# Kernel optimization log

Hardware: AMD Instinct MI355X
Metric: run time of the kernel (lower is better)

Reference implementation:

```python
import jax, jax.numpy as jnp
import numpy as np

RADIUS = 2.0  # ball-query radius (float forward arg in the original; fixed here)


def _conv1x1(x, W, b):
    # 1x1 Conv2D over NHWC == per-point linear layer
    return jnp.einsum('bmsc,cd->bmsd', x, W) + b


def _ball_query(xyz, new_xyz, radius, nsample):
    """For each cluster center, take the first (by index) nsample points within
    radius, padding with the first found neighbor (TF ball-query semantics).
    xyz: (B,N,3), new_xyz: (B,M,3) -> idx (B,M,nsample) int32."""
    N = xyz.shape[1]
    d2 = jnp.sum((new_xyz[:, :, None, :] - xyz[:, None, :, :]) ** 2, axis=-1)  # (B,M,N)
    valid = d2 < radius * radius
    key = jnp.where(valid, jnp.arange(N, dtype=jnp.int32)[None, None, :], N)
    order = jnp.argsort(key, axis=-1)[..., :nsample]          # (B,M,nsample)
    skey = jnp.take_along_axis(key, order, axis=-1)
    idx = jnp.where(skey < N, order, order[..., :1])          # pad with first neighbor
    return idx


def setup_inputs() -> dict:
    key = jax.random.key(0)
    ks = jax.random.split(key, 8)
    B, N = 8, 8192
    xyz = jax.random.normal(ks[0], (B, N, 3), dtype=jnp.float32)

    def w(k, cin, cout):
        return (jax.random.normal(k, (cin, cout), dtype=jnp.float32) / np.sqrt(cin)).astype(jnp.float32)

    z = lambda c: jnp.zeros((c,), jnp.float32)
    inp = {
        'xyz': xyz,
        'W1': w(ks[1], 3, 64),    'b1': z(64),
        'W2': w(ks[2], 64, 128),  'b2': z(128),
        'W3': w(ks[3], 128, 256), 'b3': z(256),
        'W4': w(ks[4], 256, 128), 'b4': z(128),
        'W5': w(ks[5], 128, 64),  'b5': z(64),
        'Wa': w(ks[6], 64, 1),    'ba': z(1),
        'Wo': w(ks[7], 64, 2),    'bo': z(2),
        'num_clusters': 512,
        'num_samples': 64,
    }
    return inp


def reference(xyz, W1, b1, W2, b2, W3, b3, W4, b4, W5, b5, Wa, ba, Wo, bo,
              num_clusters, num_samples):
    # sample cluster centers (deterministic stand-in for random subsampling)
    new_xyz = xyz[:, :num_clusters]                                    # (B,M,3)
    idx = _ball_query(xyz, new_xyz, RADIUS, num_samples)               # (B,M,S)
    grouped = jax.vmap(lambda pts, i: pts[i])(xyz, idx)                # (B,M,S,3)
    g = (grouped - new_xyz[:, :, None, :]) / RADIUS                    # normalize_radius

    # shared per-point MLP (1x1 convs, relu)
    h = jax.nn.relu(_conv1x1(g, W1, b1))
    h = jax.nn.relu(_conv1x1(h, W2, b2))
    h = jax.nn.relu(_conv1x1(h, W3, b3))
    # MaxPoolAxis: max over samples, keepdims
    h = jnp.max(h, axis=2, keepdims=True)                              # (B,M,1,256)
    # mlp2 convs (linear, no activation in source)
    h = _conv1x1(h, W4, b4)
    h = _conv1x1(h, W5, b5)                                            # (B,M,1,64)

    attention = jax.nn.softplus(_conv1x1(h, Wa, ba))[:, :, 0, 0]       # (B,M)
    o = _conv1x1(h, Wo, bo)[:, :, 0, :]                                # (B,M,2)
    o = o / jnp.sqrt(jnp.maximum(jnp.sum(o * o, axis=-1, keepdims=True), 1e-8))
    orientation = jnp.arctan2(o[..., 1], o[..., 0])                    # (B,M)
    return new_xyz, idx, attention, orientation
```

## Files before the change

### kernel.cpp

```cpp
#include <hip/hip_runtime.h>
#include <math.h>

#define BB 8
#define NN 8192
#define MM 512
#define SS 64
#define NCLUST (BB*MM)

#define OUT_IDX   (BB*MM*3)
#define OUT_ATT   (OUT_IDX + BB*MM*SS)
#define OUT_ORI   (OUT_ATT + BB*MM)

#define WS_W3 8192
#define WS_V  40960

typedef short v8s __attribute__((ext_vector_type(8)));
typedef float v4f __attribute__((ext_vector_type(4)));

static __device__ __forceinline__ unsigned short f2bf(float x) {
    unsigned int u = __float_as_uint(x);
    u += 0x7FFFu + ((u >> 16) & 1u);
    return (unsigned short)(u >> 16);
}

__global__ void pack_weights(const float* __restrict__ W2,
                             const float* __restrict__ W3,
                             unsigned short* __restrict__ ws)
{
    const int gid = blockIdx.x * 256 + threadIdx.x;
    const float* W; unsigned short* dst; int N, kt, nt, lane;
    if (gid < 1024) {
        W = W2; N = 128;
        const int tile = gid >> 6; lane = gid & 63;
        kt = tile >> 3; nt = tile & 7;
        dst = ws + (size_t)(tile * 64 + lane) * 8;
    } else {
        const int g = gid - 1024;
        W = W3; N = 256;
        const int tile = g >> 6; lane = g & 63;
        kt = tile >> 4; nt = tile & 15;
        dst = ws + WS_W3 + (size_t)(tile * 64 + lane) * 8;
    }
    const int k0 = kt * 32 + (lane >> 4) * 8;
    const int n  = nt * 16 + (lane & 15);
    union { unsigned short u[8]; v8s v; } f;
    #pragma unroll
    for (int j = 0; j < 8; ++j) f.u[j] = f2bf(W[(k0 + j) * N + n]);
    *(v8s*)dst = f.v;
}

__global__ __launch_bounds__(256, 4) void feat3d_front(
    const float* __restrict__ xyz,
    const float* __restrict__ W1, const float* __restrict__ b1,
    const float* __restrict__ b2, const float* __restrict__ b3,
    const unsigned short* __restrict__ Wp,
    unsigned short* __restrict__ vdst,
    float* __restrict__ out)
{
    __shared__ __align__(16) unsigned char lds[27200];
    unsigned short* a2p = (unsigned short*)lds;
    unsigned short* a3p = (unsigned short*)(lds + 8192);
    float* smallf       = (float*)(lds + 24576);
    int* ls_idx         = (int*)(lds + 26624);
    unsigned long long* ls_mask = (unsigned long long*)(lds + 26880);

    float* ls_g  = smallf;
    float* ls_w1 = smallf + 256;

    const int t   = threadIdx.x;
    const int wv  = t >> 6;
    const int l   = t & 63;
    const int q   = l >> 4;
    const int r16 = l & 15;
    const int blk = blockIdx.x;
    const int b   = blk >> 9;
    const int m   = blk & 511;
    const float* xb = xyz + (size_t)b * (NN * 3);

    const v8s* W2f = (const v8s*)Wp;
    v8s bfr[2][2];
    #pragma unroll
    for (int kt = 0; kt < 2; ++kt)
        #pragma unroll
        for (int ni = 0; ni < 2; ++ni)
            bfr[kt][ni] = W2f[(kt*8 + 2*wv + ni)*64 + l];

    const float cx = xb[m*3+0], cy = xb[m*3+1], cz = xb[m*3+2];

    if (t < 3) out[(b*MM + m)*3 + t] = xb[m*3 + t];

    if (t < 64) {
        ls_w1[t*4+0] = W1[t];
        ls_w1[t*4+1] = W1[64 + t];
        ls_w1[t*4+2] = W1[128 + t];
        ls_w1[t*4+3] = b1[t];
    }

    int cnt = 0;
    {
        int base = 0, pb = 0;
        while (base < NN && cnt < SS) {
            const int j = base + t;
            const float dx = xb[j*3+0] - cx;
            const float dy = xb[j*3+1] - cy;
            const float dz = xb[j*3+2] - cz;
            const float d2 = __fadd_rn(__fadd_rn(__fmul_rn(dx,dx), __fmul_rn(dy,dy)),
                                       __fmul_rn(dz,dz));
            const bool valid = d2 < 4.0f;
            const unsigned long long mask = __ballot(valid);
            if (l == 0) ls_mask[pb*4 + wv] = mask;
            __syncthreads();
            const unsigned long long m0 = ls_mask[pb*4+0], m1 = ls_mask[pb*4+1],
                                     m2 = ls_mask[pb*4+2], m3 = ls_mask[pb*4+3];
            int below = __popcll(mask & ((1ull << l) - 1ull));
            if (wv > 0) below += (int)__popcll(m0);
            if (wv > 1) below += (int)__popcll(m1);
            if (wv > 2) below += (int)__popcll(m2);
            const int pos = cnt + below;
            if (valid && pos < SS) {
                ls_idx[pos]   = j;
                ls_g[pos*4+0] = dx * 0.5f;
                ls_g[pos*4+1] = dy * 0.5f;
                ls_g[pos*4+2] = dz * 0.5f;
            }
            cnt += (int)(__popcll(m0) + __popcll(m1) + __popcll(m2) + __popcll(m3));
            if (cnt > SS) cnt = SS;
            base += 256;
            pb ^= 1;
        }
    }
    __syncthreads();
    if (t < SS && t >= cnt) {
        ls_idx[t]   = ls_idx[0];
        ls_g[t*4+0] = ls_g[0];
        ls_g[t*4+1] = ls_g[1];
        ls_g[t*4+2] = ls_g[2];
    }
    __syncthreads();
    if (t < 64) out[OUT_IDX + (b*MM + m)*SS + t] = (float)ls_idx[t];

    {
        const int s = wv*16 + r16;
        const float4 g4 = *(const float4*)&ls_g[s*4];
        #pragma unroll
        for (int kt = 0; kt < 2; ++kt) {
            union { unsigned short u[8]; v8s v; } fr;
            #pragma unroll
            for (int j = 0; j < 8; ++j) {
                const int c = kt*32 + q*8 + j;
                const float4 w = *(const float4*)&ls_w1[c*4];
                const float h = fmaf(g4.x, w.x, fmaf(g4.y, w.y, fmaf(g4.z, w.z, w.w)));
                fr.u[j] = f2bf(fmaxf(h, 0.f));
            }
            *(v8s*)&a2p[((kt*4 + wv)*64 + l)*8] = fr.v;
        }
    }
    __syncthreads();

    {
        const v4f z = {0.f, 0.f, 0.f, 0.f};
        v4f acc[4][2];
        #pragma unroll
        for (int mt = 0; mt < 4; ++mt) { acc[mt][0] = z; acc[mt][1] = z; }

        #pragma unroll
        for (int kt = 0; kt < 2; ++kt)
            #pragma unroll
            for (int mt = 0; mt < 4; ++mt) {
                const v8s a = *(const v8s*)&a2p[((kt*4 + mt)*64 + l)*8];
                #pragma unroll
                for (int ni = 0; ni < 2; ++ni)
                    acc[mt][ni] = __builtin_amdgcn_mfma_f32_16x16x32_bf16(
                        a, bfr[kt][ni], acc[mt][ni], 0, 0, 0);
            }

        #pragma unroll
        for (int ni = 0; ni < 2; ++ni) {
            const int c2  = (2*wv + ni)*16 + r16;
            const float bias = b2[c2];
            const int kt3 = c2 >> 5;
            const int lhi = ((c2 >> 3) & 3) << 4;
            const int j3  = c2 & 7;
            #pragma unroll
            for (int mt = 0; mt < 4; ++mt)
                #pragma unroll
                for (int rg = 0; rg < 4; ++rg) {
                    const float h = fmaxf(acc[mt][ni][rg] + bias, 0.f);
                    const int s15 = q*4 + rg;
                    a3p[((kt3*4 + mt)*64 + (lhi | s15))*8 + j3] = f2bf(h);
                }
        }
    }
    __syncthreads();

    {
        const v8s* W3f = (const v8s*)(Wp + WS_W3);
        const int cg = blk;
        unsigned short* vrow = vdst + (size_t)cg * 256;

        #pragma unroll
        for (int np = 0; np < 2; ++np) {
            const int nt0 = 4*wv + 2*np;
            const v4f z = {0.f, 0.f, 0.f, 0.f};
            v4f acc[4][2];
            #pragma unroll
            for (int mt = 0; mt < 4; ++mt) { acc[mt][0] = z; acc[mt][1] = z; }

            v8s bb0 = W3f[(0*16 + nt0    )*64 + l];
            v8s bb1 = W3f[(0*16 + nt0 + 1)*64 + l];
            #pragma unroll
            for (int kt = 0; kt < 4; ++kt) {
                v8s a[4];
                #pragma unroll
                for (int mt = 0; mt < 4; ++mt)
                    a[mt] = *(const v8s*)&a3p[((kt*4 + mt)*64 + l)*8];
                v8s nb0, nb1;
                if (kt < 3) {
                    nb0 = W3f[((kt+1)*16 + nt0    )*64 + l];
                    nb1 = W3f[((kt+1)*16 + nt0 + 1)*64 + l];
                }
                #pragma unroll
                for (int mt = 0; mt < 4; ++mt) {
                    acc[mt][0] = __builtin_amdgcn_mfma_f32_16x16x32_bf16(
                        a[mt], bb0, acc[mt][0], 0, 0, 0);
                    acc[mt][1] = __builtin_amdgcn_mfma_f32_16x16x32_bf16(
                        a[mt], bb1, acc[mt][1], 0, 0, 0);
                }
                if (kt < 3) { bb0 = nb0; bb1 = nb1; }
            }

            #pragma unroll
            for (int ni = 0; ni < 2; ++ni) {
                float mx = acc[0][ni][0];
                #pragma unroll
                for (int mt = 0; mt < 4; ++mt)
                    #pragma unroll
                    for (int rg = 0; rg < 4; ++rg)
                        mx = fmaxf(mx, acc[mt][ni][rg]);
                mx = fmaxf(mx, __shfl_xor(mx, 16));
                mx = fmaxf(mx, __shfl_xor(mx, 32));
                if (q == 0) {
                    const int c = (nt0 + ni)*16 + r16;
                    vrow[c] = f2bf(fmaxf(mx + b3[c], 0.f));
                }
            }
        }
    }
}

__global__ __launch_bounds__(256) void feat3d_tail(
    const unsigned short* __restrict__ vsrc,
    const float* __restrict__ W4, const float* __restrict__ b4,
    const float* __restrict__ W5, const float* __restrict__ b5,
    const float* __restrict__ Wa, const float* __restrict__ ba,
    const float* __restrict__ Wo, const float* __restrict__ bo,
    float* __restrict__ out)
{
    __shared__ __align__(16) float V[16][256];
    __shared__ __align__(16) float H4[16][128];
    __shared__ __align__(16) float H5[16][64];

    const int t   = threadIdx.x;
    const int cl0 = blockIdx.x * 16;

    {
        const int i  = t >> 4;
        const int ch = t & 15;
        const uint4* src = (const uint4*)(vsrc + (size_t)(cl0 + i) * 256);
        #pragma unroll
        for (int h = 0; h < 2; ++h) {
            const uint4 r = src[ch*2 + h];
            const unsigned int u[4] = {r.x, r.y, r.z, r.w};
            #pragma unroll
            for (int j = 0; j < 4; ++j) {
                V[i][ch*16 + h*8 + 2*j]     = __uint_as_float(u[j] << 16);
                V[i][ch*16 + h*8 + 2*j + 1] = __uint_as_float(u[j] & 0xFFFF0000u);
            }
        }
    }
    __syncthreads();

    {
        const int c  = t & 127;
        const int ih = t >> 7;
        float acc[8];
        #pragma unroll
        for (int i = 0; i < 8; ++i) acc[i] = b4[c];
        for (int k4 = 0; k4 < 64; ++k4) {
            const float w0 = W4[(4*k4+0)*128 + c];
            const float w1 = W4[(4*k4+1)*128 + c];
            const float w2 = W4[(4*k4+2)*128 + c];
            const float w3 = W4[(4*k4+3)*128 + c];
            #pragma unroll
            for (int i = 0; i < 8; ++i) {
                const float4 vv = *(const float4*)&V[ih*8 + i][4*k4];
                acc[i] = fmaf(vv.x, w0, fmaf(vv.y, w1,
                         fmaf(vv.z, w2, fmaf(vv.w, w3, acc[i]))));
            }
        }
        #pragma unroll
        for (int i = 0; i < 8; ++i) H4[ih*8 + i][c] = acc[i];
    }
    __syncthreads();

    {
        const int c  = t & 63;
        const int iq = t >> 6;
        float acc[4];
        #pragma unroll
        for (int i = 0; i < 4; ++i) acc[i] = b5[c];
        for (int k4 = 0; k4 < 32; ++k4) {
            const float w0 = W5[(4*k4+0)*64 + c];
            const float w1 = W5[(4*k4+1)*64 + c];
            const float w2 = W5[(4*k4+2)*64 + c];
            const float w3 = W5[(4*k4+3)*64 + c];
            #pragma unroll
            for (int i = 0; i < 4; ++i) {
                const float4 vv = *(const float4*)&H4[iq*4 + i][4*k4];
                acc[i] = fmaf(vv.x, w0, fmaf(vv.y, w1,
                         fmaf(vv.z, w2, fmaf(vv.w, w3, acc[i]))));
            }
        }
        #pragma unroll
        for (int i = 0; i < 4; ++i) H5[iq*4 + i][c] = acc[i];
    }
    __syncthreads();

    {
        const int wv = t >> 6, l = t & 63;
        const float wa  = Wa[l];
        const float wo0 = Wo[2*l + 0];
        const float wo1 = Wo[2*l + 1];
        #pragma unroll
        for (int i = 0; i < 4; ++i) {
            const float hv = H5[4*wv + i][l];
            float va = hv * wa;
            float v0 = hv * wo0;
            float v1 = hv * wo1;
            #pragma unroll
            for (int off = 32; off > 0; off >>= 1) {
                va += __shfl_down(va, off);
                v0 += __shfl_down(v0, off);
                v1 += __shfl_down(v1, off);
            }
            if (l == 0) {
                const int cg = cl0 + 4*wv + i;
                const float a = va + ba[0];
                out[OUT_ATT + cg] = fmaxf(a, 0.f) + log1pf(expf(-fabsf(a)));
                out[OUT_ORI + cg] = atan2f(v1 + bo[1], v0 + bo[0]);
            }
        }
    }
}

extern "C" void kernel_launch(void* const* d_in, const int* in_sizes, int n_in,
                              void* d_out, int out_size, void* d_ws, size_t ws_size,
                              hipStream_t stream) {
    const float* xyz = (const float*)d_in[0];
    const float* W1  = (const float*)d_in[1];
    const float* b1  = (const float*)d_in[2];
    const float* W2  = (const float*)d_in[3];
    const float* b2  = (const float*)d_in[4];
    const float* W3  = (const float*)d_in[5];
    const float* b3  = (const float*)d_in[6];
    const float* W4  = (const float*)d_in[7];
    const float* b4  = (const float*)d_in[8];
    const float* W5  = (const float*)d_in[9];
    const float* b5  = (const float*)d_in[10];
    const float* Wa  = (const float*)d_in[11];
    const float* ba  = (const float*)d_in[12];
    const float* Wo  = (const float*)d_in[13];
    const float* bo  = (const float*)d_in[14];

    unsigned short* ws = (unsigned short*)d_ws;

    pack_weights<<<dim3(20), dim3(256), 0, stream>>>(W2, W3, ws);
    feat3d_front<<<dim3(NCLUST), dim3(256), 0, stream>>>(
        xyz, W1, b1, b2, b3, ws, ws + WS_V, (float*)d_out);
    feat3d_tail<<<dim3(NCLUST/16), dim3(256), 0, stream>>>(
        ws + WS_V, W4, b4, W5, b5, Wa, ba, Wo, bo, (float*)d_out);
}
```

Measured before the change: 138.8 us.

## Fuse tail MLP into per-cluster front kernel, dropping intermediate buffer and launch

```diff
diff --git a/kernel.cpp b/kernel.cpp
--- a/kernel.cpp
+++ b/kernel.cpp
@@ -12,7 +12,6 @@
 #define OUT_ORI   (OUT_ATT + BB*MM)
 
 #define WS_W3 8192
-#define WS_V  40960
 
 typedef short v8s __attribute__((ext_vector_type(8)));
 typedef float v4f __attribute__((ext_vector_type(4)));
@@ -49,12 +48,15 @@
     *(v8s*)dst = f.v;
 }
 
-__global__ __launch_bounds__(256, 4) void feat3d_front(
+__global__ __launch_bounds__(256, 4) void feat3d_fused(
     const float* __restrict__ xyz,
     const float* __restrict__ W1, const float* __restrict__ b1,
     const float* __restrict__ b2, const float* __restrict__ b3,
     const unsigned short* __restrict__ Wp,
-    unsigned short* __restrict__ vdst,
+    const float* __restrict__ W4, const float* __restrict__ b4,
+    const float* __restrict__ W5, const float* __restrict__ b5,
+    const float* __restrict__ Wa, const float* __restrict__ ba,
+    const float* __restrict__ Wo, const float* __restrict__ bo,
     float* __restrict__ out)
 {
     __shared__ __align__(16) unsigned char lds[27200];
@@ -66,6 +68,11 @@
 
     float* ls_g  = smallf;
     float* ls_w1 = smallf + 256;
+
+    float* vbuf = (float*)lds;
+    float* h4p  = (float*)(lds + 1024);
+    float* h4f  = (float*)(lds + 2048);
+    float* h5p  = (float*)(lds + 2560);
 
     const int t   = threadIdx.x;
     const int wv  = t >> 6;
@@ -195,8 +202,6 @@
 
     {
         const v8s* W3f = (const v8s*)(Wp + WS_W3);
-        const int cg = blk;
-        unsigned short* vrow = vdst + (size_t)cg * 256;
 
         #pragma unroll
         for (int np = 0; np < 2; ++np) {
@@ -241,114 +246,62 @@
                 mx = fmaxf(mx, __shfl_xor(mx, 32));
                 if (q == 0) {
                     const int c = (nt0 + ni)*16 + r16;
-                    vrow[c] = f2bf(fmaxf(mx + b3[c], 0.f));
+                    vbuf[c] = fmaxf(mx + b3[c], 0.f);
                 }
             }
         }
     }
-}
-
-__global__ __launch_bounds__(256) void feat3d_tail(
-    const unsigned short* __restrict__ vsrc,
-    const float* __restrict__ W4, const float* __restrict__ b4,
-    const float* __restrict__ W5, const float* __restrict__ b5,
-    const float* __restrict__ Wa, const float* __restrict__ ba,
-    const float* __restrict__ Wo, const float* __restrict__ bo,
-    float* __restrict__ out)
-{
-    __shared__ __align__(16) float V[16][256];
-    __shared__ __align__(16) float H4[16][128];
-    __shared__ __align__(16) float H5[16][64];
-
-    const int t   = threadIdx.x;
-    const int cl0 = blockIdx.x * 16;
-
-    {
-        const int i  = t >> 4;
-        const int ch = t & 15;
-        const uint4* src = (const uint4*)(vsrc + (size_t)(cl0 + i) * 256);
-        #pragma unroll
-        for (int h = 0; h < 2; ++h) {
-            const uint4 r = src[ch*2 + h];
-            const unsigned int u[4] = {r.x, r.y, r.z, r.w};
-            #pragma unroll
-            for (int j = 0; j < 4; ++j) {
-                V[i][ch*16 + h*8 + 2*j]     = __uint_as_float(u[j] << 16);
-                V[i][ch*16 + h*8 + 2*j + 1] = __uint_as_float(u[j] & 0xFFFF0000u);
-            }
-        }
-    }
-    __syncthreads();
-
-    {
-        const int c  = t & 127;
-        const int ih = t >> 7;
-        float acc[8];
-        #pragma unroll
-        for (int i = 0; i < 8; ++i) acc[i] = b4[c];
-        for (int k4 = 0; k4 < 64; ++k4) {
-            const float w0 = W4[(4*k4+0)*128 + c];
-            const float w1 = W4[(4*k4+1)*128 + c];
-            const float w2 = W4[(4*k4+2)*128 + c];
-            const float w3 = W4[(4*k4+3)*128 + c];
-            #pragma unroll
-            for (int i = 0; i < 8; ++i) {
-                const float4 vv = *(const float4*)&V[ih*8 + i][4*k4];
-                acc[i] = fmaf(vv.x, w0, fmaf(vv.y, w1,
-                         fmaf(vv.z, w2, fmaf(vv.w, w3, acc[i]))));
-            }
-        }
-        #pragma unroll
-        for (int i = 0; i < 8; ++i) H4[ih*8 + i][c] = acc[i];
-    }
-    __syncthreads();
-
-    {
-        const int c  = t & 63;
-        const int iq = t >> 6;
-        float acc[4];
-        #pragma unroll
-        for (int i = 0; i < 4; ++i) acc[i] = b5[c];
-        for (int k4 = 0; k4 < 32; ++k4) {
-            const float w0 = W5[(4*k4+0)*64 + c];
-            const float w1 = W5[(4*k4+1)*64 + c];
-            const float w2 = W5[(4*k4+2)*64 + c];
-            const float w3 = W5[(4*k4+3)*64 + c];
-            #pragma unroll
-            for (int i = 0; i < 4; ++i) {
-                const float4 vv = *(const float4*)&H4[iq*4 + i][4*k4];
-                acc[i] = fmaf(vv.x, w0, fmaf(vv.y, w1,
-                         fmaf(vv.z, w2, fmaf(vv.w, w3, acc[i]))));
-            }
-        }
-        #pragma unroll
-        for (int i = 0; i < 4; ++i) H5[iq*4 + i][c] = acc[i];
-    }
-    __syncthreads();
-
-    {
-        const int wv = t >> 6, l = t & 63;
-        const float wa  = Wa[l];
-        const float wo0 = Wo[2*l + 0];
-        const float wo1 = Wo[2*l + 1];
-        #pragma unroll
-        for (int i = 0; i < 4; ++i) {
-            const float hv = H5[4*wv + i][l];
-            float va = hv * wa;
-            float v0 = hv * wo0;
-            float v1 = hv * wo1;
-            #pragma unroll
-            for (int off = 32; off > 0; off >>= 1) {
-                va += __shfl_down(va, off);
-                v0 += __shfl_down(v0, off);
-                v1 += __shfl_down(v1, off);
-            }
-            if (l == 0) {
-                const int cg = cl0 + 4*wv + i;
-                const float a = va + ba[0];
-                out[OUT_ATT + cg] = fmaxf(a, 0.f) + log1pf(expf(-fabsf(a)));
-                out[OUT_ORI + cg] = atan2f(v1 + bo[1], v0 + bo[0]);
-            }
+    __syncthreads();
+
+    {
+        const int c4 = t & 127;
+        const int kh = t >> 7;
+        const float* W4c = W4 + c4;
+        float acc = 0.f;
+        for (int k = kh*128; k < kh*128 + 128; k += 4) {
+            const float4 vv = *(const float4*)&vbuf[k];
+            acc = fmaf(vv.x, W4c[(k+0)*128],
+                  fmaf(vv.y, W4c[(k+1)*128],
+                  fmaf(vv.z, W4c[(k+2)*128],
+                  fmaf(vv.w, W4c[(k+3)*128], acc))));
+        }
+        h4p[t] = acc;
+    }
+    __syncthreads();
+    if (t < 128) h4f[t] = h4p[t] + h4p[128 + t] + b4[t];
+    __syncthreads();
+
+    {
+        const int c5 = t & 63;
+        const int kq = t >> 6;
+        const float* W5c = W5 + c5;
+        float acc = 0.f;
+        for (int k = kq*32; k < kq*32 + 32; k += 4) {
+            const float4 hh = *(const float4*)&h4f[k];
+            acc = fmaf(hh.x, W5c[(k+0)*64],
+                  fmaf(hh.y, W5c[(k+1)*64],
+                  fmaf(hh.z, W5c[(k+2)*64],
+                  fmaf(hh.w, W5c[(k+3)*64], acc))));
+        }
+        h5p[t] = acc;
+    }
+    __syncthreads();
+
+    if (t < 64) {
+        const float h5v = h5p[t] + h5p[64 + t] + h5p[128 + t] + h5p[192 + t] + b5[t];
+        float va = h5v * Wa[t];
+        float v0 = h5v * Wo[2*t + 0];
+        float v1 = h5v * Wo[2*t + 1];
+        #pragma unroll
+        for (int off = 32; off > 0; off >>= 1) {
+            va += __shfl_down(va, off);
+            v0 += __shfl_down(v0, off);
+            v1 += __shfl_down(v1, off);
+        }
+        if (t == 0) {
+            const float a = va + ba[0];
+            out[OUT_ATT + blk] = fmaxf(a, 0.f) + log1pf(expf(-fabsf(a)));
+            out[OUT_ORI + blk] = atan2f(v1 + bo[1], v0 + bo[0]);
         }
     }
 }
@@ -375,8 +328,6 @@
     unsigned short* ws = (unsigned short*)d_ws;
 
     pack_weights<<<dim3(20), dim3(256), 0, stream>>>(W2, W3, ws);
-    feat3d_front<<<dim3(NCLUST), dim3(256), 0, stream>>>(
-        xyz, W1, b1, b2, b3, ws, ws + WS_V, (float*)d_out);
-    feat3d_tail<<<dim3(NCLUST/16), dim3(256), 0, stream>>>(
-        ws + WS_V, W4, b4, W5, b5, Wa, ba, Wo, bo, (float*)d_out);
+    feat3d_fused<<<dim3(NCLUST), dim3(256), 0, stream>>>(
+        xyz, W1, b1, b2, b3, ws, W4, b4, W5, b5, Wa, ba, Wo, bo, (float*)d_out);
 }
```

New measurement: 134.3 us. 1.03x faster.
